# Kernel tuning notes

Hardware: AMD Instinct MI355X
Metric: run time of the kernel (lower is better)

## Reference

```python
import jax, jax.numpy as jnp
import numpy as np

B, T, IDIM, HDIM, K, LMAX, NLAYERS = 64, 1024, 120, 320, 72, 96, 3
LAMB = 0.1
NEG = -1e30


def lse3(a, b, c):
    m = jnp.maximum(jnp.maximum(a, b), c)
    return m + jnp.log(jnp.exp(a - m) + jnp.exp(b - m) + jnp.exp(c - m))


def _lstm_dir(x, Wih, Whh, bb):
    # x: [B,T,D] -> h: [B,T,H]; PyTorch gate order i,f,g,o
    gx = jnp.einsum('btd,gd->tbg', x, Wih) + bb  # [T,B,4H]
    def step(carry, g):
        h, c = carry
        g = g + h @ Whh.T
        i, f, gg, o = jnp.split(g, 4, axis=-1)
        c = jax.nn.sigmoid(f) * c + jax.nn.sigmoid(i) * jnp.tanh(gg)
        h = jax.nn.sigmoid(o) * jnp.tanh(c)
        return (h, c), h
    h0 = jnp.zeros((x.shape[0], HDIM), x.dtype)
    _, hs = jax.lax.scan(step, (h0, h0), gx)
    return hs.transpose(1, 0, 2)


def _rev(x, lengths):
    # reverse each sequence within its valid length (packed-sequence semantics)
    t = jnp.arange(x.shape[1])
    idx = jnp.where(t[None, :] < lengths[:, None], lengths[:, None] - 1 - t[None, :], t[None, :])
    return jnp.take_along_axis(x, idx[:, :, None], axis=1)


def _blstm_layer(x, Wih_f, Whh_f, b_f, Wih_b, Whh_b, b_b, lengths):
    hf = _lstm_dir(x, Wih_f, Whh_f, b_f)
    hb = _rev(_lstm_dir(_rev(x, lengths), Wih_b, Whh_b, b_b), lengths)
    return jnp.concatenate([hf, hb], axis=2)


def _ctc_forward(logp, labels, in_lens, lab_lens):
    # standard CTC alpha recursion (blank=0), log-space, vectorized over batch
    Bn, Tn, _ = logp.shape
    S = 2 * LMAX + 1
    ext = jnp.zeros((Bn, S), jnp.int32).at[:, 1::2].set(labels)  # blank-interleaved labels
    em = jnp.take_along_axis(logp, jnp.broadcast_to(ext[:, None, :], (Bn, Tn, S)), axis=2)
    em = em.transpose(1, 0, 2)  # [T,B,S]
    s_idx = jnp.arange(S)
    prev_lab = jnp.concatenate([jnp.full((Bn, 2), -1, jnp.int32), ext[:, :-2]], axis=1)
    can_skip = ((s_idx[None, :] % 2) == 1) & (ext != prev_lab)
    valid_s = s_idx[None, :] < (2 * lab_lens[:, None] + 1)
    alpha0 = jnp.full((Bn, S), NEG, logp.dtype)
    alpha0 = alpha0.at[:, 0].set(em[0][:, 0]).at[:, 1].set(em[0][:, 1])
    alpha0 = jnp.where(valid_s, alpha0, NEG)
    def step(alpha, inp):
        em_t, t = inp
        a2 = jnp.concatenate([jnp.full((Bn, 1), NEG, alpha.dtype), alpha[:, :-1]], axis=1)
        a3 = jnp.concatenate([jnp.full((Bn, 2), NEG, alpha.dtype), alpha[:, :-2]], axis=1)
        a3 = jnp.where(can_skip, a3, NEG)
        new = lse3(alpha, a2, a3) + em_t
        new = jnp.where(valid_s, new, NEG)
        new = jnp.where((t < in_lens)[:, None], new, alpha)  # freeze past utterance end
        return new, None
    alpha, _ = jax.lax.scan(step, alpha0, (em[1:], jnp.arange(1, Tn)))
    last = 2 * lab_lens
    aL = jnp.take_along_axis(alpha, last[:, None], axis=1)[:, 0]
    aLm1 = jnp.take_along_axis(alpha, (last - 1)[:, None], axis=1)[:, 0]
    return jnp.logaddexp(aL, aLm1)  # log p(labels | x)


def setup_inputs():
    key = jax.random.key(0)
    ks = jax.random.split(key, 12)
    H4 = 4 * HDIM
    s = 0.05
    return dict(
        logits=jax.random.normal(ks[0], (B, T, IDIM), jnp.float32),
        labels_padded=jax.random.randint(ks[1], (B, LMAX), 1, K).astype(jnp.int32),
        input_lengths=jax.random.randint(ks[2], (B,), T // 2, T + 1).astype(jnp.int32),
        label_lengths=jax.random.randint(ks[3], (B,), LMAX // 2, LMAX + 1).astype(jnp.int32),
        Wih0=jax.random.normal(ks[4], (2, H4, IDIM), jnp.float32) * s,
        Whh0=jax.random.normal(ks[5], (2, H4, HDIM), jnp.float32) * s,
        b0=jnp.zeros((2, H4), jnp.float32),
        Wih=jax.random.normal(ks[6], (NLAYERS - 1, 2, H4, 2 * HDIM), jnp.float32) * s,
        Whh=jax.random.normal(ks[7], (NLAYERS - 1, 2, H4, HDIM), jnp.float32) * s,
        b=jnp.zeros((NLAYERS - 1, 2, H4), jnp.float32),
        W_lin=jax.random.normal(ks[8], (K, 2 * HDIM), jnp.float32) * s,
        b_lin=jnp.zeros((K,), jnp.float32),
    )


def reference(logits, labels_padded, input_lengths, label_lengths, Wih0, Whh0, b0, Wih, Whh, b, W_lin, b_lin):
    # sort by input length descending (mirrors torch.sort + index_select)
    order = jnp.argsort(-input_lengths)
    logits = logits[order]
    labels_padded = labels_padded[order]
    input_lengths = input_lengths[order]
    label_lengths = label_lengths[order]
    # 3-layer BLSTM encoder
    x = _blstm_layer(logits, Wih0[0], Whh0[0], b0[0], Wih0[1], Whh0[1], b0[1], input_lengths)
    for l in range(NLAYERS - 1):
        x = _blstm_layer(x, Wih[l, 0], Whh[l, 0], b[l, 0], Wih[l, 1], Whh[l, 1], b[l, 1], input_lengths)
    netout = jax.nn.log_softmax(x @ W_lin.T + b_lin, axis=2)  # [B,T,K]
    # CTC-CRF: numerator = CTC alpha log-prob; denominator = free-running partition
    num = _ctc_forward(netout, labels_padded, input_lengths, label_lengths)
    tmask = jnp.arange(netout.shape[1])[None, :] < input_lengths[:, None]
    den = jnp.sum(jnp.where(tmask, jax.nn.logsumexp(netout, axis=2), 0.0), axis=1)
    return jnp.mean(den - (1.0 + LAMB) * num)
```

## Files before the change

### kernel.cpp

```cpp
#include <hip/hip_runtime.h>
#include <cstdint>
#include <cstddef>


typedef _Float16 f16;
typedef _Float16 h2v   __attribute__((ext_vector_type(2)));
typedef _Float16 f16x4v __attribute__((ext_vector_type(4)));
typedef _Float16 f16x8 __attribute__((ext_vector_type(8)));
typedef float    f32x4 __attribute__((ext_vector_type(4)));
typedef uint32_t u32x4 __attribute__((ext_vector_type(4)));

#define NEGF (-1e30f)
#define CT 128

__device__ __forceinline__ float dot2f(h2v a, h2v b, float c) {
#if __has_builtin(__builtin_amdgcn_fdot2)
  return __builtin_amdgcn_fdot2(a, b, c, false);
#else
  return c + (float)a.x * (float)b.x + (float)a.y * (float)b.y;
#endif
}

__device__ __forceinline__ float fast_rcp(float x) {
#if __has_builtin(__builtin_amdgcn_rcpf)
  return __builtin_amdgcn_rcpf(x);
#else
  return 1.f / x;
#endif
}
__device__ __forceinline__ float fsigm(float x) { return fast_rcp(1.f + __expf(-x)); }
__device__ __forceinline__ float ftanh(float x) { return 1.f - 2.f * fast_rcp(1.f + __expf(2.f * x)); }

__device__ __forceinline__ void stage16(f16* lds, const f16* g) {
#if __has_builtin(__builtin_amdgcn_global_load_lds)
  __builtin_amdgcn_global_load_lds(
      (const __attribute__((address_space(1))) uint32_t*)g,
      (__attribute__((address_space(3))) uint32_t*)lds, 16, 0, 0);
#else
  int lane = threadIdx.x & 63;
  *(f16x8*)&lds[lane * 8] = *(const f16x8*)g;
#endif
}


__global__ void conv_logits(const float* __restrict__ src, f16* __restrict__ dst) {
  int idx = blockIdx.x * 256 + threadIdx.x;
  int row = idx >> 7, k = idx & 127;
  dst[idx] = (f16)((k < 120) ? src[(size_t)row * 120 + k] : 0.f);
}

__global__ void conv_wt0(const float* __restrict__ w, f16* __restrict__ dst) {
  int idx = blockIdx.x * 256 + threadIdx.x;
  int n = idx >> 7, k = idx & 127;
  dst[idx] = (f16)((k < 120) ? w[(size_t)n * 120 + k] : 0.f);
}

__global__ void conv_copy(const float* __restrict__ src, f16* __restrict__ dst, int count) {
  int idx = blockIdx.x * 256 + threadIdx.x;
  if (idx < count) dst[idx] = (f16)src[idx];
}

__global__ void conv_wtl(const float* __restrict__ w, f16* __restrict__ dst) {
  int idx = blockIdx.x * 256 + threadIdx.x;
  int n = idx / 640, k = idx % 640;
  dst[idx] = (f16)((n < 72) ? w[(size_t)n * 640 + k] : 0.f);
}

__global__ void conv_whh(const float* __restrict__ whh0, const float* __restrict__ whh,
                         uint32_t* __restrict__ dst) {
  int o = blockIdx.x * 256 + threadIdx.x;
  int tid = o & 511;
  int g  = o >> 9;
  int j  = g % 40;
  int g2 = g / 40;
  int i  = g2 % 5;
  int g3 = g2 / 5;
  int hf = g3 & 1, slot = g3 >> 1;
  int tau = i * 512 + tid;
  int lr = tau >> 2, kq = tau & 3;
  int gate = lr / 160, u = lr - gate * 160;
  int r = gate * 320 + hf * 160 + u;
  int k = kq * 80 + j * 2;
  const float* srcm = (slot < 2) ? (whh0 + ((size_t)slot * 1280 + r) * 320)
                                 : (whh  + ((size_t)(slot - 2) * 1280 + r) * 320);
  f16 lo = (f16)srcm[k], hi = (f16)srcm[k + 1];
  dst[o] = (uint32_t)__builtin_bit_cast(unsigned short, lo) |
           ((uint32_t)__builtin_bit_cast(unsigned short, hi) << 16);
}

__global__ __launch_bounds__(256)
void gemm_chunk(const f16* __restrict__ A, const f16* __restrict__ W,
                f16* __restrict__ gxc, const int* __restrict__ lens,
                int lda, int kTiles, int c0) {
  __shared__ __align__(16) f16 As[128 * 32];
  __shared__ __align__(16) f16 Ws[2][128 * 32];
  const int tid = threadIdx.x;
  const int lane = tid & 63, wid = tid >> 6;
  const int wm = wid >> 1, wn = wid & 1;
  const int dir = blockIdx.y >> 6, b = blockIdx.y & 63;
  const int n0 = blockIdx.x * 256;
  const int r_base = lane >> 2;
  const int chs = ((((lane & 3) + (r_base >> 1)) & 3)) * 8;
  const int len = lens[b];

  f32x4 acc[4][8] = {};

  for (int kt = 0; kt < kTiles; ++kt) {
    const int k0 = kt * 32;
    __syncthreads();
#pragma unroll
    for (int hh = 0; hh < 2; ++hh) {
      const int c = wid * 2 + hh;
      const int j = c * 16 + r_base;
      const int s = c0 * CT + j;
      const int tt = dir ? ((s < len) ? (len - 1 - s) : s) : s;
      stage16(&As[c * 512], A + (size_t)(b * 1024 + tt) * lda + k0 + chs);
    }
#pragma unroll
    for (int hh = 0; hh < 4; ++hh) {
      const int c = wid * 4 + hh;
      const int tile = c >> 3, cc = c & 7;
      stage16(&Ws[tile][cc * 512],
              W + (size_t)(dir * 1280 + n0 + tile * 128 + cc * 16 + r_base) * lda + k0 + chs);
    }
    __syncthreads();

    const int q = lane >> 4;
    const int l15 = lane & 15;
    const int cs = (q - (l15 >> 1)) & 3;
    const int rofs = l15 * 32 + cs * 8;
    f16x8 av[4], wv0[4], wv1[4];
#pragma unroll
    for (int i = 0; i < 4; ++i)
      av[i] = *(const f16x8*)&As[(wm * 4 + i) * 512 + rofs];
#pragma unroll
    for (int i = 0; i < 4; ++i) {
      wv0[i] = *(const f16x8*)&Ws[0][(wn * 4 + i) * 512 + rofs];
      wv1[i] = *(const f16x8*)&Ws[1][(wn * 4 + i) * 512 + rofs];
    }
#pragma unroll
    for (int i = 0; i < 4; ++i)
#pragma unroll
      for (int j = 0; j < 4; ++j) {
        acc[i][j]     = __builtin_amdgcn_mfma_f32_16x16x32_f16(av[i], wv0[j], acc[i][j], 0, 0, 0);
        acc[i][4 + j] = __builtin_amdgcn_mfma_f32_16x16x32_f16(av[i], wv1[j], acc[i][4 + j], 0, 0, 0);
      }
  }

  const int r0 = (lane >> 4) * 4, cn = lane & 15;
  const size_t obase = (size_t)(dir * 64 + b) * CT;
#pragma unroll
  for (int i = 0; i < 4; ++i) {
    const int m = wm * 64 + i * 16 + r0;
#pragma unroll
    for (int j = 0; j < 4; ++j) {
      const int n = n0 + wn * 64 + j * 16 + cn;
#pragma unroll
      for (int r = 0; r < 4; ++r) {
        gxc[(obase + m + r) * 1280 + n]       = (f16)acc[i][j][r];
        gxc[(obase + m + r) * 1280 + n + 128] = (f16)acc[i][4 + j][r];
      }
    }
  }
}

__global__ void __launch_bounds__(512)
__attribute__((amdgpu_waves_per_eu(2, 2)))
lstm_scan_chunk(const volatile uint32_t* wbuf,
                const f16* __restrict__ gxc,
                const float* __restrict__ bias,
                const int* __restrict__ lens,
                f16* xnext,
                uint32_t* xq,
                f16* hsave,
                float* csave,
                int layer, int c0) {
  const int wg = blockIdx.x;
  const int half = wg >> 7;
  const int bd = wg & 127;
  const int b = bd >> 1, dir = bd & 1;
  const int tid = threadIdx.x;

  __shared__ __align__(16) f16 hbuf[320];
  __shared__ float ylds[640];
  __shared__ __align__(16) f16 hstage[64 * 160];

  h2v w[5][40];
  {
    const volatile uint32_t* wb =
        wbuf + (size_t)((layer * 2 + dir) * 2 + half) * 200 * 512;
#pragma unroll
    for (int i = 0; i < 5; ++i)
#pragma unroll
      for (int j = 0; j < 40; ++j) {
        uint32_t v = wb[(i * 40 + j) * 512 + tid];
        w[i][j] = __builtin_bit_cast(h2v, v);
      }
  }
  if (tid < 320) hbuf[tid] = (c0 == 0) ? (f16)0.f : hsave[bd * 320 + tid];

  const int len = lens[b];
  const int kq = tid & 3;
  const int qi = tid >> 2;
  const int gu = half * 160 + tid;
  float c_state = 0.f;
  float bi = 0.f, bff = 0.f, bg = 0.f, bo = 0.f;
  if (tid < 160) {
    if (c0 > 0) c_state = csave[wg * 160 + tid];
    const float* bp = bias + dir * 1280 + gu;
    bi = bp[0]; bff = bp[320]; bg = bp[640]; bo = bp[960];
  }
  __syncthreads();

  const size_t grow0 = (size_t)(dir * 64 + b) * CT;

  float gxi = 0.f, gxf = 0.f, gxg = 0.f, gxo = 0.f;
  if (tid < 160) {
    const f16* gp = gxc + grow0 * 1280 + gu;
    gxi = (float)gp[0]; gxf = (float)gp[320]; gxg = (float)gp[640]; gxo = (float)gp[960];
  }

  for (int tl = 0; tl < CT; ++tl) {
    const int s = c0 * CT + tl;
    const uint32_t tag = (uint32_t)(layer * 1024 + s + 1);

    float nxi = 0.f, nxf = 0.f, nxg = 0.f, nxo = 0.f;
    if (tid < 160 && tl + 1 < CT) {
      const f16* gp = gxc + (grow0 + tl + 1) * 1280 + gu;
      nxi = (float)gp[0]; nxf = (float)gp[320]; nxg = (float)gp[640]; nxo = (float)gp[960];
    }

    float a0 = 0.f, a1 = 0.f, a2 = 0.f, a3 = 0.f, a4 = 0.f;
    {
      const u32x4* h4 = (const u32x4*)hbuf;
#pragma unroll
      for (int jb = 0; jb < 5; ++jb) {
        u32x4 p = h4[kq * 10 + jb * 2];
        u32x4 q = h4[kq * 10 + jb * 2 + 1];
        h2v hr[8];
#pragma unroll
        for (int j = 0; j < 4; ++j) hr[j] = __builtin_bit_cast(h2v, p[j]);
#pragma unroll
        for (int j = 0; j < 4; ++j) hr[4 + j] = __builtin_bit_cast(h2v, q[j]);
#pragma unroll
        for (int j = 0; j < 8; ++j) {
          a0 = dot2f(w[0][jb * 8 + j], hr[j], a0);
          a1 = dot2f(w[1][jb * 8 + j], hr[j], a1);
          a2 = dot2f(w[2][jb * 8 + j], hr[j], a2);
          a3 = dot2f(w[3][jb * 8 + j], hr[j], a3);
          a4 = dot2f(w[4][jb * 8 + j], hr[j], a4);
        }
      }
    }
    {
      float av[5] = {a0, a1, a2, a3, a4};
#pragma unroll
      for (int i = 0; i < 5; ++i) {
        float v = av[i];
        v += __shfl_xor(v, 1, 64);
        v += __shfl_xor(v, 2, 64);
        if (kq == 0) ylds[i * 128 + qi] = v;
      }
    }

    if ((tl & 31) == 0 && tl > 0) {
      const int tw = tl - 32;
#pragma unroll
      for (int it = 0; it < 2; ++it) {
        const int slot = it * 512 + tid;
        if (slot < 640) {
          const int r = (int)(((unsigned)slot * 52429u) >> 20);
          const int j = slot - r * 20;
          const int sp = c0 * CT + tw + r;
          const int ttp = dir ? ((sp < len) ? (len - 1 - sp) : sp) : sp;
          f16x8 v = *(const f16x8*)&hstage[((tw + r) & 63) * 160 + j * 8];
          *(f16x8*)&xnext[(size_t)(b * 1024 + ttp) * 640 + dir * 320 + half * 160 + j * 8] = v;
        }
      }
    }
    __syncthreads();

    if (tid < 160) {
      const int u = tid;
      float pi = ylds[u]       + gxi + bi;
      float pf = ylds[160 + u] + gxf + bff;
      float pg = ylds[320 + u] + gxg + bg;
      float po = ylds[480 + u] + gxo + bo;
      float ig = fsigm(pi);
      float fg = fsigm(pf);
      float gg = ftanh(pg);
      float og = fsigm(po);
      c_state = fg * c_state + ig * gg;
      float hv = og * ftanh(c_state);
      const f16 hh = (f16)hv;
      const uint32_t word = (tag << 16) |
                            (uint32_t)__builtin_bit_cast(unsigned short, hh);
      __hip_atomic_exchange(&xq[((bd * 2 + half) * 2 + (s & 1)) * 160 + u], word,
                            __ATOMIC_RELAXED, __HIP_MEMORY_SCOPE_AGENT);
      hbuf[gu] = hh;
      hstage[(tl & 63) * 160 + u] = hh;
    } else if (tid >= 256 && tid < 416) {
      const int u = tid - 256;
      uint32_t pw;
      int spins = 0;
      do {
        pw = __hip_atomic_fetch_add(&xq[((bd * 2 + (1 - half)) * 2 + (s & 1)) * 160 + u],
                                    0u, __ATOMIC_RELAXED, __HIP_MEMORY_SCOPE_AGENT);
      } while ((pw >> 16) != tag && ++spins < 30000);
      hbuf[(1 - half) * 160 + u] =
          __builtin_bit_cast(f16, (unsigned short)(pw & 0xffffu));
    }
    __syncthreads();

    gxi = nxi; gxf = nxf; gxg = nxg; gxo = nxo;
  }

  {
    const int tw = CT - 32;
#pragma unroll
    for (int it = 0; it < 2; ++it) {
      const int slot = it * 512 + tid;
      if (slot < 640) {
        const int r = (int)(((unsigned)slot * 52429u) >> 20);
        const int j = slot - r * 20;
        const int sp = c0 * CT + tw + r;
        const int ttp = dir ? ((sp < len) ? (len - 1 - sp) : sp) : sp;
        f16x8 v = *(const f16x8*)&hstage[((tw + r) & 63) * 160 + j * 8];
        *(f16x8*)&xnext[(size_t)(b * 1024 + ttp) * 640 + dir * 320 + half * 160 + j * 8] = v;
      }
    }
  }
  if (tid < 160) {
    hsave[bd * 320 + gu] = hbuf[gu];
    csave[wg * 160 + tid] = c_state;
  }
}

__global__ __launch_bounds__(256)
void gemm_proj(const f16* __restrict__ A, const f16* __restrict__ W,
               float* __restrict__ outf, int lda, int kTiles, int ldo) {
  __shared__ __align__(16) f16 As[128 * 32];
  __shared__ __align__(16) f16 Ws[128 * 32];
  const int tid = threadIdx.x;
  const int lane = tid & 63, wid = tid >> 6;
  const int wm = wid >> 1, wn = wid & 1;
  const int m0 = blockIdx.y * 128, n0 = blockIdx.x * 128;
  const int r_base = lane >> 2;
  const int chs = ((((lane & 3) + (r_base >> 1)) & 3)) * 8;

  f32x4 acc[4][4] = {};

  for (int kt = 0; kt < kTiles; ++kt) {
    const int k0 = kt * 32;
    __syncthreads();
#pragma unroll
    for (int hh = 0; hh < 2; ++hh) {
      const int c = wid * 2 + hh;
      stage16(&As[c * 512], A + (size_t)(m0 + c * 16 + r_base) * lda + k0 + chs);
      stage16(&Ws[c * 512], W + (size_t)(n0 + c * 16 + r_base) * lda + k0 + chs);
    }
    __syncthreads();

    const int q = lane >> 4;
    const int l15 = lane & 15;
    const int cs = (q - (l15 >> 1)) & 3;
    const int rofs = l15 * 32 + cs * 8;
    f16x8 av[4], wv[4];
#pragma unroll
    for (int i = 0; i < 4; ++i)
      av[i] = *(const f16x8*)&As[(wm * 4 + i) * 512 + rofs];
#pragma unroll
    for (int i = 0; i < 4; ++i)
      wv[i] = *(const f16x8*)&Ws[(wn * 4 + i) * 512 + rofs];
#pragma unroll
    for (int i = 0; i < 4; ++i)
#pragma unroll
      for (int j = 0; j < 4; ++j)
        acc[i][j] = __builtin_amdgcn_mfma_f32_16x16x32_f16(av[i], wv[j], acc[i][j], 0, 0, 0);
  }

  const int r0 = (lane >> 4) * 4, cn = lane & 15;
#pragma unroll
  for (int i = 0; i < 4; ++i) {
    const int m = m0 + wm * 64 + i * 16 + r0;
#pragma unroll
    for (int j = 0; j < 4; ++j) {
      const int n = n0 + wn * 64 + j * 16 + cn;
#pragma unroll
      for (int r = 0; r < 4; ++r)
        outf[(size_t)(m + r) * ldo + n] = acc[i][j][r];
    }
  }
}

__global__ void lse_kernel(const float* __restrict__ Z, const float* __restrict__ b_lin,
                           float* __restrict__ lseout) {
  int row = blockIdx.x * 4 + (threadIdx.x >> 6);
  int l = threadIdx.x & 63;
  const float* z = Z + (size_t)row * 128;
  float v0 = (l < 72) ? z[l] + b_lin[l] : NEGF;
  float v1 = (l < 8) ? z[l + 64] + b_lin[l + 64] : NEGF;
  float m = fmaxf(v0, v1);
#pragma unroll
  for (int o = 32; o; o >>= 1) m = fmaxf(m, __shfl_xor(m, o, 64));
  float s = ((l < 72) ? __expf(v0 - m) : 0.f) + ((l < 8) ? __expf(v1 - m) : 0.f);
#pragma unroll
  for (int o = 32; o; o >>= 1) s += __shfl_xor(s, o, 64);
  if (l == 0) lseout[row] = m + __logf(s);
}

__global__ void emz_kernel(const float* __restrict__ Z, const float* __restrict__ lse,
                           const float* __restrict__ b_lin,
                           const int* __restrict__ labels,
                           f16* __restrict__ emc) {
  const int b = blockIdx.y;
  const int t0 = blockIdx.x * 4;
  const int tid = threadIdx.x;
  __shared__ int ext[200];
  __shared__ float bls[200];
  if (tid < 200) {
    int e = (tid < 193 && (tid & 1)) ? labels[b * 96 + (tid >> 1)] : 0;
    ext[tid] = e;
    bls[tid] = b_lin[e];
  }
  __syncthreads();
#pragma unroll
  for (int dt = 0; dt < 4; ++dt) {
    const int t = t0 + dt;
    const float lst = lse[b * 1024 + t];
    const float* zr = Z + ((size_t)(b * 1024 + t)) * 128;
    for (int s = tid; s < 200; s += 256)
      emc[((size_t)(b * 1024 + t)) * 200 + s] = (f16)(zr[ext[s]] + bls[s] - lst);
  }
}

__global__ void ctc_kernel(const f16* __restrict__ emc,
                           const int* __restrict__ labels, const int* __restrict__ inlen,
                           const int* __restrict__ lablen, float* __restrict__ num) {
  const int b = blockIdx.x;
  const int lane = threadIdx.x;
  __shared__ int ext[200];
  __shared__ float afin[200];

  for (int s = lane; s < 200; s += 64)
    ext[s] = (s < 193 && (s & 1)) ? labels[b * 96 + (s >> 1)] : 0;
  __syncthreads();

  const int L = lablen[b], len = inlen[b];
  const int Send = 2 * L + 1;
  const f16* eb = emc + (size_t)b * 1024 * 200;

  float a[4];
  bool  skp[4], val[4];
#pragma unroll
  for (int j = 0; j < 4; ++j) {
    const int s = lane * 4 + j;
    val[j] = (s < Send) && (s < 193);
    skp[j] = (s < 193) && (s & 1) && (s >= 2) && (ext[s] != ext[s - 2]);
  }
  {
    f16x4v e0 = *(const f16x4v*)&eb[lane * 4];
#pragma unroll
    for (int j = 0; j < 4; ++j) {
      const int s = lane * 4 + j;
      a[j] = (s <= 1 && val[j]) ? (float)e0[j] : NEGF;
    }
  }

  auto step = [&](f16x4v ev) {
    float p3 = __shfl_up(a[3], 1, 64);
    float p2 = __shfl_up(a[2], 1, 64);
    if (lane == 0) { p3 = NEGF; p2 = NEGF; }
    const float x2[4] = {p3, a[0], a[1], a[2]};
    const float x3[4] = {p2, p3, a[0], a[1]};
#pragma unroll
    for (int j = 0; j < 4; ++j) {
      const float xa = a[j], xb = x2[j];
      const float xc = skp[j] ? x3[j] : NEGF;
      const float m = fmaxf(xa, fmaxf(xb, xc));
      const float sum = __expf(xa - m) + __expf(xb - m) + __expf(xc - m);
      const float nv = m + __logf(sum) + (float)ev[j];
      a[j] = val[j] ? nv : NEGF;
    }
  };

  f16x4v ring[4];
#pragma unroll
  for (int d = 1; d <= 4; ++d) {
    const int r = (d < len) ? d : (len - 1);
    ring[d & 3] = *(const f16x4v*)&eb[(size_t)r * 200 + lane * 4];
  }

  int t = 1;
  for (; t + 4 <= len; t += 4) {
#pragma unroll
    for (int k = 0; k < 4; ++k) {
      const int slot = (1 + k) & 3;
      f16x4v ev = ring[slot];
      const int tp = t + k + 4;
      if (tp < len)
        ring[slot] = *(const f16x4v*)&eb[(size_t)tp * 200 + lane * 4];
      step(ev);
    }
  }
  for (; t < len; ++t)
    step(*(const f16x4v*)&eb[(size_t)t * 200 + lane * 4]);

#pragma unroll
  for (int j = 0; j < 4; ++j) {
    const int s = lane * 4 + j;
    if (s < 193) afin[s] = a[j];
  }
  __syncthreads();
  if (lane == 0) {
    const float aL = afin[2 * L], aLm1 = afin[2 * L - 1];
    const float m = fmaxf(aL, aLm1);
    num[b] = m + __logf(__expf(aL - m) + __expf(aLm1 - m));
  }
}

__global__ void final_kernel(const float* __restrict__ num, float* __restrict__ out) {
  int l = threadIdx.x;
  float v = -1.1f * num[l];
#pragma unroll
  for (int o = 32; o; o >>= 1) v += __shfl_xor(v, o, 64);
  if (l == 0) out[0] = v * (1.f / 64.f);
}

__global__ void sentinel_kernel(float* __restrict__ out, float code) { out[0] = code; }

extern "C" void kernel_launch(void* const* d_in, const int* in_sizes, int n_in,
                              void* d_out, int out_size, void* d_ws, size_t ws_size,
                              hipStream_t stream) {
  (void)in_sizes; (void)n_in; (void)out_size;

  const float* logits   = (const float*)d_in[0];
  const int*   labels   = (const int*)d_in[1];
  const int*   in_lens  = (const int*)d_in[2];
  const int*   lab_lens = (const int*)d_in[3];
  const float* Wih0     = (const float*)d_in[4];
  const float* Whh0     = (const float*)d_in[5];
  const float* b0       = (const float*)d_in[6];
  const float* Wih      = (const float*)d_in[7];
  const float* Whh      = (const float*)d_in[8];
  const float* bb       = (const float*)d_in[9];
  const float* W_lin    = (const float*)d_in[10];
  const float* b_lin    = (const float*)d_in[11];

  const size_t NEED = (size_t)224 * 1024 * 1024;
  if (ws_size < NEED) {
    sentinel_kernel<<<1, 1, 0, stream>>>((float*)d_out, -(float)(ws_size >> 20));
    return;
  }

  char* ws = (char*)d_ws;
  size_t off = 0;
  auto alloc = [&](size_t bytes) -> char* {
    char* p = ws + off;
    off += (bytes + 255) & ~(size_t)255;
    return p;
  };
  f16*      Xa     = (f16*)alloc((size_t)65536 * 640 * 2);
  f16*      Xb     = (f16*)alloc((size_t)65536 * 640 * 2);
  f16*      gxc    = (f16*)alloc((size_t)2 * 64 * CT * 1280 * 2);
  f16*      Wt0    = (f16*)alloc((size_t)2560 * 128 * 2);
  f16*      Wt12   = (f16*)alloc((size_t)2 * 2560 * 640 * 2);
  f16*      WtL    = (f16*)alloc((size_t)128 * 640 * 2);
  uint32_t* whh16  = (uint32_t*)alloc((size_t)6 * 2 * 200 * 512 * 4);
  float*    lseb   = (float*)alloc((size_t)65536 * 4);
  float*    num    = (float*)alloc(64 * 4);
  uint32_t* xq     = (uint32_t*)alloc((size_t)512 * 160 * 4);
  f16*      hsave  = (f16*)alloc((size_t)128 * 320 * 2);
  float*    csave  = (float*)alloc((size_t)256 * 160 * 4);
  f16*      A0     = Xb;
  float*    Z      = (float*)gxc;
  f16*      emc    = Xa;

  hipMemsetAsync(xq, 0, (size_t)512 * 160 * 4, stream);

  conv_logits<<<32768, 256, 0, stream>>>(logits, A0);
  conv_wt0<<<1280, 256, 0, stream>>>(Wih0, Wt0);
  conv_copy<<<12800, 256, 0, stream>>>(Wih, Wt12, 3276800);
  conv_wtl<<<320, 256, 0, stream>>>(W_lin, WtL);
  conv_whh<<<4800, 256, 0, stream>>>(Whh0, Whh, whh16);

  for (int c = 0; c < 1024 / CT; ++c) {
    gemm_chunk<<<dim3(5, 128), 256, 0, stream>>>(A0, Wt0, gxc, in_lens, 128, 4, c);
    lstm_scan_chunk<<<256, 512, 0, stream>>>(whh16, gxc, b0, in_lens, Xa, xq,
                                             hsave, csave, 0, c);
  }
  for (int c = 0; c < 1024 / CT; ++c) {
    gemm_chunk<<<dim3(5, 128), 256, 0, stream>>>(Xa, Wt12, gxc, in_lens, 640, 20, c);
    lstm_scan_chunk<<<256, 512, 0, stream>>>(whh16, gxc, bb, in_lens, Xb, xq,
                                             hsave, csave, 1, c);
  }
  for (int c = 0; c < 1024 / CT; ++c) {
    gemm_chunk<<<dim3(5, 128), 256, 0, stream>>>(Xb, Wt12 + (size_t)2560 * 640, gxc,
                                                 in_lens, 640, 20, c);
    lstm_scan_chunk<<<256, 512, 0, stream>>>(whh16, gxc, bb + 2560, in_lens, Xa, xq,
                                             hsave, csave, 2, c);
  }
  gemm_proj<<<dim3(1, 512), 256, 0, stream>>>(Xa, WtL, Z, 640, 20, 128);

  lse_kernel<<<16384, 256, 0, stream>>>(Z, b_lin, lseb);
  emz_kernel<<<dim3(256, 64), 256, 0, stream>>>(Z, lseb, b_lin, labels, emc);
  ctc_kernel<<<64, 64, 0, stream>>>(emc, labels, in_lens, lab_lens, num);
  final_kernel<<<1, 64, 0, stream>>>(num, (float*)d_out);
}
```

Measured before the change: 9.000 ms.

## Add fast L2 polling path for LSTM halves and base-2 CTC with deeper prefetch

The cross-workgroup h exchange now writes each word to a second buffer with a plain workgroup-scope store, which the consumer polls with an sc0 global load before falling back to agent-scope atomic loads on the original buffer. The producer's atomic exchange becomes an atomic store. This targets the latency of the per-step handoff between the two workgroups that split each LSTM cell. Separately, CTC emissions are pre-scaled to base 2 so the recursion uses native exp2/log2, and the emission prefetch ring grows from 4 to 8 steps. The fast path relies on undocumented cache-visibility behaviour and adds a duplicate store per step.

```diff
diff --git a/kernel.cpp b/kernel.cpp
--- a/kernel.cpp
+++ b/kernel.cpp
@@ -30,6 +30,31 @@
 }
 __device__ __forceinline__ float fsigm(float x) { return fast_rcp(1.f + __expf(-x)); }
 __device__ __forceinline__ float ftanh(float x) { return 1.f - 2.f * fast_rcp(1.f + __expf(2.f * x)); }
+
+__device__ __forceinline__ float fexp2(float x) {
+#if __has_builtin(__builtin_amdgcn_exp2f)
+  return __builtin_amdgcn_exp2f(x);
+#else
+  return exp2f(x);
+#endif
+}
+__device__ __forceinline__ float flog2(float x) {
+#if __has_builtin(__builtin_amdgcn_logf)
+  return __builtin_amdgcn_logf(x);
+#else
+  return log2f(x);
+#endif
+}
+
+__device__ __forceinline__ uint32_t poll_l2(const uint32_t* p) {
+  uint32_t v;
+  asm volatile("global_load_dword %0, %1, off sc0\n\t"
+               "s_waitcnt vmcnt(0)"
+               : "=&v"(v)
+               : "v"(p)
+               : "memory");
+  return v;
+}
 
 __device__ __forceinline__ void stage16(f16* lds, const f16* g) {
 #if __has_builtin(__builtin_amdgcn_global_load_lds)
@@ -172,6 +197,7 @@
                 const int* __restrict__ lens,
                 f16* xnext,
                 uint32_t* xq,
+                uint32_t* xqf,
                 f16* hsave,
                 float* csave,
                 int layer, int c0) {
@@ -219,6 +245,8 @@
     const f16* gp = gxc + grow0 * 1280 + gu;
     gxi = (float)gp[0]; gxf = (float)gp[320]; gxg = (float)gp[640]; gxo = (float)gp[960];
   }
+
+  int fastmiss = 0;
 
   for (int tl = 0; tl < CT; ++tl) {
     const int s = c0 * CT + tl;
@@ -295,18 +323,33 @@
       const f16 hh = (f16)hv;
       const uint32_t word = (tag << 16) |
                             (uint32_t)__builtin_bit_cast(unsigned short, hh);
-      __hip_atomic_exchange(&xq[((bd * 2 + half) * 2 + (s & 1)) * 160 + u], word,
-                            __ATOMIC_RELAXED, __HIP_MEMORY_SCOPE_AGENT);
+      const int qidx = ((bd * 2 + half) * 2 + (s & 1)) * 160 + u;
+      __hip_atomic_store(&xqf[qidx], word, __ATOMIC_RELAXED,
+                         __HIP_MEMORY_SCOPE_WORKGROUP);
+      __hip_atomic_store(&xq[qidx], word, __ATOMIC_RELAXED,
+                         __HIP_MEMORY_SCOPE_AGENT);
       hbuf[gu] = hh;
       hstage[(tl & 63) * 160 + u] = hh;
     } else if (tid >= 256 && tid < 416) {
       const int u = tid - 256;
-      uint32_t pw;
-      int spins = 0;
-      do {
-        pw = __hip_atomic_fetch_add(&xq[((bd * 2 + (1 - half)) * 2 + (s & 1)) * 160 + u],
-                                    0u, __ATOMIC_RELAXED, __HIP_MEMORY_SCOPE_AGENT);
-      } while ((pw >> 16) != tag && ++spins < 30000);
+      const int qidx = ((bd * 2 + (1 - half)) * 2 + (s & 1)) * 160 + u;
+      uint32_t pw = 0;
+      bool got = false;
+      if (fastmiss < 2) {
+        int tries = 16;
+        do {
+          pw = poll_l2(&xqf[qidx]);
+        } while ((pw >> 16) != tag && --tries);
+        got = ((pw >> 16) == tag);
+        fastmiss = got ? 0 : (fastmiss + 1);
+      }
+      if (!got) {
+        int spins = 0;
+        do {
+          pw = __hip_atomic_load(&xq[qidx], __ATOMIC_RELAXED,
+                                 __HIP_MEMORY_SCOPE_AGENT);
+        } while ((pw >> 16) != tag && ++spins < 200000);
+      }
       hbuf[(1 - half) * 160 + u] =
           __builtin_bit_cast(f16, (unsigned short)(pw & 0xffffu));
     }
@@ -430,7 +473,8 @@
     const float lst = lse[b * 1024 + t];
     const float* zr = Z + ((size_t)(b * 1024 + t)) * 128;
     for (int s = tid; s < 200; s += 256)
-      emc[((size_t)(b * 1024 + t)) * 200 + s] = (f16)(zr[ext[s]] + bls[s] - lst);
+      emc[((size_t)(b * 1024 + t)) * 200 + s] =
+          (f16)((zr[ext[s]] + bls[s] - lst) * 1.4426950408889634f);
   }
 }
 
@@ -478,26 +522,26 @@
       const float xa = a[j], xb = x2[j];
       const float xc = skp[j] ? x3[j] : NEGF;
       const float m = fmaxf(xa, fmaxf(xb, xc));
-      const float sum = __expf(xa - m) + __expf(xb - m) + __expf(xc - m);
-      const float nv = m + __logf(sum) + (float)ev[j];
+      const float sum = fexp2(xa - m) + fexp2(xb - m) + fexp2(xc - m);
+      const float nv = m + flog2(sum) + (float)ev[j];
       a[j] = val[j] ? nv : NEGF;
     }
   };
 
-  f16x4v ring[4];
-#pragma unroll
-  for (int d = 1; d <= 4; ++d) {
+  f16x4v ring[8];
+#pragma unroll
+  for (int d = 1; d <= 8; ++d) {
     const int r = (d < len) ? d : (len - 1);
-    ring[d & 3] = *(const f16x4v*)&eb[(size_t)r * 200 + lane * 4];
+    ring[d & 7] = *(const f16x4v*)&eb[(size_t)r * 200 + lane * 4];
   }
 
   int t = 1;
-  for (; t + 4 <= len; t += 4) {
-#pragma unroll
-    for (int k = 0; k < 4; ++k) {
-      const int slot = (1 + k) & 3;
+  for (; t + 8 <= len; t += 8) {
+#pragma unroll
+    for (int k = 0; k < 8; ++k) {
+      const int slot = (1 + k) & 7;
       f16x4v ev = ring[slot];
-      const int tp = t + k + 4;
+      const int tp = t + k + 8;
       if (tp < len)
         ring[slot] = *(const f16x4v*)&eb[(size_t)tp * 200 + lane * 4];
       step(ev);
@@ -515,7 +559,7 @@
   if (lane == 0) {
     const float aL = afin[2 * L], aLm1 = afin[2 * L - 1];
     const float m = fmaxf(aL, aLm1);
-    num[b] = m + __logf(__expf(aL - m) + __expf(aLm1 - m));
+    num[b] = 0.6931471805599453f * (m + flog2(fexp2(aL - m) + fexp2(aLm1 - m)));
   }
 }
 
@@ -570,6 +614,7 @@
   float*    lseb   = (float*)alloc((size_t)65536 * 4);
   float*    num    = (float*)alloc(64 * 4);
   uint32_t* xq     = (uint32_t*)alloc((size_t)512 * 160 * 4);
+  uint32_t* xqf    = (uint32_t*)alloc((size_t)512 * 160 * 4);
   f16*      hsave  = (f16*)alloc((size_t)128 * 320 * 2);
   float*    csave  = (float*)alloc((size_t)256 * 160 * 4);
   f16*      A0     = Xb;
@@ -577,6 +622,7 @@
   f16*      emc    = Xa;
 
   hipMemsetAsync(xq, 0, (size_t)512 * 160 * 4, stream);
+  hipMemsetAsync(xqf, 0, (size_t)512 * 160 * 4, stream);
 
   conv_logits<<<32768, 256, 0, stream>>>(logits, A0);
   conv_wt0<<<1280, 256, 0, stream>>>(Wih0, Wt0);
@@ -586,18 +632,18 @@
 
   for (int c = 0; c < 1024 / CT; ++c) {
     gemm_chunk<<<dim3(5, 128), 256, 0, stream>>>(A0, Wt0, gxc, in_lens, 128, 4, c);
-    lstm_scan_chunk<<<256, 512, 0, stream>>>(whh16, gxc, b0, in_lens, Xa, xq,
+    lstm_scan_chunk<<<256, 512, 0, stream>>>(whh16, gxc, b0, in_lens, Xa, xq, xqf,
                                              hsave, csave, 0, c);
   }
   for (int c = 0; c < 1024 / CT; ++c) {
     gemm_chunk<<<dim3(5, 128), 256, 0, stream>>>(Xa, Wt12, gxc, in_lens, 640, 20, c);
-    lstm_scan_chunk<<<256, 512, 0, stream>>>(whh16, gxc, bb, in_lens, Xb, xq,
+    lstm_scan_chunk<<<256, 512, 0, stream>>>(whh16, gxc, bb, in_lens, Xb, xq, xqf,
                                              hsave, csave, 1, c);
   }
   for (int c = 0; c < 1024 / CT; ++c) {
     gemm_chunk<<<dim3(5, 128), 256, 0, stream>>>(Xb, Wt12 + (size_t)2560 * 640, gxc,
                                                  in_lens, 640, 20, c);
-    lstm_scan_chunk<<<256, 512, 0, stream>>>(whh16, gxc, bb + 2560, in_lens, Xa, xq,
+    lstm_scan_chunk<<<256, 512, 0, stream>>>(whh16, gxc, bb + 2560, in_lens, Xa, xq, xqf,
                                              hsave, csave, 2, c);
   }
   gemm_proj<<<dim3(1, 512), 256, 0, stream>>>(Xa, WtL, Z, 640, 20, 128);
```

New measurement: 8.897 ms. Within noise of the previous version (-1.1%).
